# Kernel tuning notes

Hardware: AMD Instinct MI355X
Metric: run time of the kernel (lower is better)

## Reference

```python
import jax, jax.numpy as jnp
import numpy as np

B, N = 8, 256
IN_F, OUT_F = 64, 64
IN_E, OUT_E = 32, 64  # out_edges must equal out_features (batched matmul constraint)


def setup_inputs() -> dict:
    key = jax.random.key(0)
    ks = jax.random.split(key, 9)
    s = 0.05
    return {
        "A": jax.random.uniform(ks[0], (B, N, N), dtype=jnp.float32),
        "emb_node": jax.random.normal(ks[1], (B, N, IN_F), dtype=jnp.float32),
        "emb_edge": jax.random.normal(ks[2], (B, N, N, IN_E), dtype=jnp.float32),
        "W_node": jax.random.normal(ks[3], (IN_F, OUT_F), dtype=jnp.float32) * s,
        "b_node": jnp.zeros((OUT_F,), dtype=jnp.float32),
        "W_nodes": jax.random.normal(ks[4], (IN_F, OUT_F), dtype=jnp.float32) * s,
        "b_nodes": jnp.zeros((OUT_F,), dtype=jnp.float32),
        "W_edge": jax.random.normal(ks[5], (IN_E, OUT_E), dtype=jnp.float32) * s,
        "b_edge": jnp.zeros((OUT_E,), dtype=jnp.float32),
    }


def reference(A, emb_node, emb_edge, W_node, b_node, W_nodes, b_nodes, W_edge, b_edge):
    # Dense projections (last-axis matmul, like keras Dense)
    node_x = emb_node @ W_node + b_node        # [B,N,F]
    node_sx = emb_node @ W_nodes + b_nodes     # [B,N,F]
    edge_x = emb_edge @ W_edge + b_edge        # [B,N,N,E] (E == F)
    # Fused edge-weighted aggregation: original materializes A[...,None]*edge_x
    # then does a per-channel batched matmul with node_x; same math as:
    #   node_out[b,n,f] = sum_m A[b,n,m] * edge_x[b,n,m,f] * node_x[b,m,f]
    agg = jnp.einsum('bnm,bnmf,bmf->bnf', A, edge_x, node_x)
    node_out = jax.nn.relu(agg) + jax.nn.relu(node_sx)
    edge_out = jax.nn.relu(edge_x)
    return node_out, edge_out
```

## Files before the change

kernel.cpp:

```cpp
#include <hip/hip_runtime.h>

#define BB    8
#define NN    256
#define INF   64
#define OUTF  64
#define INE   32
#define OUTE  64

using f4 = __attribute__((ext_vector_type(4))) float;

__device__ float g_node_x[BB * NN * OUTF];
__device__ float g_relu_sx[BB * NN * OUTF];

__global__ __launch_bounds__(256) void node_proj(
    const float* __restrict__ emb_node,
    const float* __restrict__ W1, const float* __restrict__ b1,
    const float* __restrict__ W2, const float* __restrict__ b2)
{
    __shared__ float sW1[64][64];
    __shared__ float sW2[64][64];
    __shared__ float sE[4][64];

    const int tid = threadIdx.x;

    const f4* w1v = (const f4*)W1;
    const f4* w2v = (const f4*)W2;
    f4* s1 = (f4*)&sW1[0][0];
    f4* s2 = (f4*)&sW2[0][0];
#pragma unroll
    for (int i = 0; i < 4; ++i) {
        s1[tid + i * 256] = w1v[tid + i * 256];
        s2[tid + i * 256] = w2v[tid + i * 256];
    }
    const int row0 = blockIdx.x * 4;
    if (tid < 64) ((f4*)&sE[0][0])[tid] = ((const f4*)(emb_node + row0 * 64))[tid];
    __syncthreads();

    const int s = tid >> 6;
    const int f = tid & 63;
    float a1 = b1[f];
    float a2 = b2[f];
#pragma unroll
    for (int k = 0; k < 64; ++k) {
        const float e = sE[s][k];
        a1 = fmaf(e, sW1[k][f], a1);
        a2 = fmaf(e, sW2[k][f], a2);
    }
    const int row = row0 + s;
    g_node_x[row * 64 + f]  = a1;
    g_relu_sx[row * 64 + f] = fmaxf(a2, 0.f);
}

__global__ __launch_bounds__(512, 4) void edge_agg(
    const float* __restrict__ A,
    const float* __restrict__ emb_edge,
    const float* __restrict__ W_edge,
    const float* __restrict__ b_edge,
    float* __restrict__ node_out,
    float* __restrict__ edge_out)
{
    __shared__ float sE[256][36];
    __shared__ float sW[32][64];
    __shared__ float sA[256];
    __shared__ float sRed[32][64];

    const int tid = threadIdx.x;
    const int bn  = blockIdx.x;
    const int b   = bn >> 8;

    const float* embBase = emb_edge + (size_t)bn * (NN * INE);
#pragma unroll
    for (int it = 0; it < 4; ++it) {
        const int i  = tid + it * 512;
        const f4   v = __builtin_nontemporal_load(((const f4*)embBase) + i);
        const int m  = i >> 3;
        const int k4 = i & 7;
        *(f4*)&sE[m][k4 * 4] = v;
    }
    ((f4*)&sW[0][0])[tid] = ((const f4*)W_edge)[tid];
    if (tid < 64) ((f4*)sA)[tid] = ((const f4*)(A + bn * NN))[tid];
    __syncthreads();

    const int fg = tid & 15;
    const int mg = tid >> 4;
    const int f0 = fg * 4;

    const f4 bias = *(const f4*)(b_edge + f0);
    float acc[8][4];
#pragma unroll
    for (int i = 0; i < 8; ++i) {
        acc[i][0] = bias.x; acc[i][1] = bias.y; acc[i][2] = bias.z; acc[i][3] = bias.w;
    }

#pragma unroll
    for (int k4 = 0; k4 < 8; ++k4) {
        f4 ev[8];
#pragma unroll
        for (int i = 0; i < 8; ++i)
            ev[i] = *(const f4*)&sE[mg + i * 32][k4 * 4];
#pragma unroll
        for (int kk = 0; kk < 4; ++kk) {
            const f4 w = *(const f4*)&sW[k4 * 4 + kk][f0];
#pragma unroll
            for (int i = 0; i < 8; ++i) {
                const float e = (kk == 0) ? ev[i].x
                              : (kk == 1) ? ev[i].y
                              : (kk == 2) ? ev[i].z
                                          : ev[i].w;
                acc[i][0] = fmaf(e, w.x, acc[i][0]);
                acc[i][1] = fmaf(e, w.y, acc[i][1]);
                acc[i][2] = fmaf(e, w.z, acc[i][2]);
                acc[i][3] = fmaf(e, w.w, acc[i][3]);
            }
        }
    }

    const float* nx = g_node_x + b * (NN * OUTF);
    const size_t outBase = (size_t)bn * (NN * OUTE);
    float agg0 = 0.f, agg1 = 0.f, agg2 = 0.f, agg3 = 0.f;
#pragma unroll
    for (int i = 0; i < 8; ++i) {
        const int m = mg + i * 32;
        const float a = sA[m];
        const f4 nxv = *(const f4*)&nx[m * 64 + f0];
        f4 st;
        st.x = fmaxf(acc[i][0], 0.f);
        st.y = fmaxf(acc[i][1], 0.f);
        st.z = fmaxf(acc[i][2], 0.f);
        st.w = fmaxf(acc[i][3], 0.f);
        __builtin_nontemporal_store(st, (f4*)&edge_out[outBase + (size_t)m * 64 + f0]);
        agg0 = fmaf(a * acc[i][0], nxv.x, agg0);
        agg1 = fmaf(a * acc[i][1], nxv.y, agg1);
        agg2 = fmaf(a * acc[i][2], nxv.z, agg2);
        agg3 = fmaf(a * acc[i][3], nxv.w, agg3);
    }
    f4 aggv; aggv.x = agg0; aggv.y = agg1; aggv.z = agg2; aggv.w = agg3;
    *(f4*)&sRed[mg][f0] = aggv;
    __syncthreads();

    if (tid < 64) {
        float s = 0.f;
#pragma unroll
        for (int g = 0; g < 32; ++g) s += sRed[g][tid];
        node_out[bn * 64 + tid] = fmaxf(s, 0.f) + g_relu_sx[bn * 64 + tid];
    }
}

extern "C" void kernel_launch(void* const* d_in, const int* in_sizes, int n_in,
                              void* d_out, int out_size, void* d_ws, size_t ws_size,
                              hipStream_t stream) {
    const float* A        = (const float*)d_in[0];
    const float* emb_node = (const float*)d_in[1];
    const float* emb_edge = (const float*)d_in[2];
    const float* W_node   = (const float*)d_in[3];
    const float* b_node   = (const float*)d_in[4];
    const float* W_nodes  = (const float*)d_in[5];
    const float* b_nodes  = (const float*)d_in[6];
    const float* W_edge   = (const float*)d_in[7];
    const float* b_edge   = (const float*)d_in[8];

    float* node_out = (float*)d_out;
    float* edge_out = node_out + BB * NN * OUTF;

    node_proj<<<(BB * NN) / 4, 256, 0, stream>>>(emb_node, W_node, b_node, W_nodes, b_nodes);
    edge_agg<<<BB * NN, 512, 0, stream>>>(A, emb_edge, W_edge, b_edge, node_out, edge_out);
}
```

Before: 53.82 us.

## Compute edge projection with bf16 MFMA instead of FP32 FMAs

Converts the edge embeddings and a transposed copy of W_edge to bf16 in shared memory, then computes the 256x64 per-row projection with 16x16x32 bf16 MFMA instructions. The epilogue is restructured around the MFMA output layout: scalar nontemporal stores, and a wave-level shuffle reduction before a smaller cross-wave shared reduction. This is meant to cut ALU time and LDS traffic in the edge kernel. The risks are reduced precision from rounding inputs to bf16 and narrower store instructions.

```diff
diff --git a/kernel.cpp b/kernel.cpp
--- a/kernel.cpp
+++ b/kernel.cpp
@@ -7,10 +7,19 @@
 #define INE   32
 #define OUTE  64
 
-using f4 = __attribute__((ext_vector_type(4))) float;
+using f4     = __attribute__((ext_vector_type(4))) float;
+using f32x4  = __attribute__((ext_vector_type(4))) float;
+using bf16x8 = __attribute__((ext_vector_type(8))) short;
+using us4    = __attribute__((ext_vector_type(4))) unsigned short;
 
 __device__ float g_node_x[BB * NN * OUTF];
 __device__ float g_relu_sx[BB * NN * OUTF];
+
+static __device__ __forceinline__ unsigned short f2bf(float x) {
+    unsigned u = __builtin_bit_cast(unsigned, x);
+    u += 0x7fffu + ((u >> 16) & 1u);
+    return (unsigned short)(u >> 16);
+}
 
 __global__ __launch_bounds__(256) void node_proj(
     const float* __restrict__ emb_node,
@@ -59,89 +68,104 @@
     float* __restrict__ node_out,
     float* __restrict__ edge_out)
 {
-    __shared__ float sE[256][36];
-    __shared__ float sW[32][64];
+    __shared__ unsigned short sEb[256][32];
+    __shared__ unsigned short sWt[64][32];
     __shared__ float sA[256];
-    __shared__ float sRed[32][64];
+    __shared__ float sRed[8][64];
 
     const int tid = threadIdx.x;
     const int bn  = blockIdx.x;
     const int b   = bn >> 8;
 
-    const float* embBase = emb_edge + (size_t)bn * (NN * INE);
+    const f4* embv = (const f4*)(emb_edge + (size_t)bn * (NN * INE));
 #pragma unroll
     for (int it = 0; it < 4; ++it) {
-        const int i  = tid + it * 512;
-        const f4   v = __builtin_nontemporal_load(((const f4*)embBase) + i);
-        const int m  = i >> 3;
-        const int k4 = i & 7;
-        *(f4*)&sE[m][k4 * 4] = v;
+        const int i = tid + it * 512;
+        const f4 v = __builtin_nontemporal_load(embv + i);
+        us4 h;
+        h.x = f2bf(v.x); h.y = f2bf(v.y); h.z = f2bf(v.z); h.w = f2bf(v.w);
+        *(us4*)&sEb[i >> 3][(i & 7) * 4] = h;
     }
-    ((f4*)&sW[0][0])[tid] = ((const f4*)W_edge)[tid];
+    {
+        const int f  = tid >> 3;
+        const int k0 = (tid & 7) * 4;
+        us4 h;
+        h.x = f2bf(W_edge[(k0 + 0) * 64 + f]);
+        h.y = f2bf(W_edge[(k0 + 1) * 64 + f]);
+        h.z = f2bf(W_edge[(k0 + 2) * 64 + f]);
+        h.w = f2bf(W_edge[(k0 + 3) * 64 + f]);
+        *(us4*)&sWt[f][k0] = h;
+    }
     if (tid < 64) ((f4*)sA)[tid] = ((const f4*)(A + bn * NN))[tid];
+
+    const int wave  = tid >> 6;
+    const int lane  = tid & 63;
+    const int lrow  = lane >> 4;
+    const int lcol  = lane & 15;
+    const int mbase = wave * 32;
+
+    float bias[4];
+#pragma unroll
+    for (int ft = 0; ft < 4; ++ft) bias[ft] = b_edge[ft * 16 + lcol];
+
     __syncthreads();
 
-    const int fg = tid & 15;
-    const int mg = tid >> 4;
-    const int f0 = fg * 4;
+    bf16x8 afrag[2];
+#pragma unroll
+    for (int mt = 0; mt < 2; ++mt)
+        afrag[mt] = *(const bf16x8*)&sEb[mbase + mt * 16 + lcol][lrow * 8];
+    bf16x8 bfrag[4];
+#pragma unroll
+    for (int ft = 0; ft < 4; ++ft)
+        bfrag[ft] = *(const bf16x8*)&sWt[ft * 16 + lcol][lrow * 8];
 
-    const f4 bias = *(const f4*)(b_edge + f0);
-    float acc[8][4];
+    f32x4 acc[2][4];
 #pragma unroll
-    for (int i = 0; i < 8; ++i) {
-        acc[i][0] = bias.x; acc[i][1] = bias.y; acc[i][2] = bias.z; acc[i][3] = bias.w;
-    }
+    for (int mt = 0; mt < 2; ++mt)
+#pragma unroll
+        for (int ft = 0; ft < 4; ++ft) {
+            f32x4 c; c[0] = bias[ft]; c[1] = bias[ft]; c[2] = bias[ft]; c[3] = bias[ft];
+            acc[mt][ft] = __builtin_amdgcn_mfma_f32_16x16x32_bf16(
+                afrag[mt], bfrag[ft], c, 0, 0, 0);
+        }
 
+    const float* nx = g_node_x + b * (NN * OUTF);
+    float* eoutBase = edge_out + (size_t)bn * (NN * OUTE);
+    float agg[4] = {0.f, 0.f, 0.f, 0.f};
 #pragma unroll
-    for (int k4 = 0; k4 < 8; ++k4) {
-        f4 ev[8];
+    for (int mt = 0; mt < 2; ++mt) {
 #pragma unroll
-        for (int i = 0; i < 8; ++i)
-            ev[i] = *(const f4*)&sE[mg + i * 32][k4 * 4];
+        for (int r = 0; r < 4; ++r) {
+            const int m = mbase + mt * 16 + lrow * 4 + r;
+            const float a = sA[m];
+            const float* nxr = nx + m * 64 + lcol;
+            float* er = eoutBase + (size_t)m * 64 + lcol;
 #pragma unroll
-        for (int kk = 0; kk < 4; ++kk) {
-            const f4 w = *(const f4*)&sW[k4 * 4 + kk][f0];
-#pragma unroll
-            for (int i = 0; i < 8; ++i) {
-                const float e = (kk == 0) ? ev[i].x
-                              : (kk == 1) ? ev[i].y
-                              : (kk == 2) ? ev[i].z
-                                          : ev[i].w;
-                acc[i][0] = fmaf(e, w.x, acc[i][0]);
-                acc[i][1] = fmaf(e, w.y, acc[i][1]);
-                acc[i][2] = fmaf(e, w.z, acc[i][2]);
-                acc[i][3] = fmaf(e, w.w, acc[i][3]);
+            for (int ft = 0; ft < 4; ++ft) {
+                const float v = acc[mt][ft][r];
+                __builtin_nontemporal_store(fmaxf(v, 0.f), er + ft * 16);
+                agg[ft] = fmaf(a * v, nxr[ft * 16], agg[ft]);
             }
         }
     }
 
-    const float* nx = g_node_x + b * (NN * OUTF);
-    const size_t outBase = (size_t)bn * (NN * OUTE);
-    float agg0 = 0.f, agg1 = 0.f, agg2 = 0.f, agg3 = 0.f;
 #pragma unroll
-    for (int i = 0; i < 8; ++i) {
-        const int m = mg + i * 32;
-        const float a = sA[m];
-        const f4 nxv = *(const f4*)&nx[m * 64 + f0];
-        f4 st;
-        st.x = fmaxf(acc[i][0], 0.f);
-        st.y = fmaxf(acc[i][1], 0.f);
-        st.z = fmaxf(acc[i][2], 0.f);
-        st.w = fmaxf(acc[i][3], 0.f);
-        __builtin_nontemporal_store(st, (f4*)&edge_out[outBase + (size_t)m * 64 + f0]);
-        agg0 = fmaf(a * acc[i][0], nxv.x, agg0);
-        agg1 = fmaf(a * acc[i][1], nxv.y, agg1);
-        agg2 = fmaf(a * acc[i][2], nxv.z, agg2);
-        agg3 = fmaf(a * acc[i][3], nxv.w, agg3);
+    for (int ft = 0; ft < 4; ++ft) {
+        float v = agg[ft];
+        v += __shfl_xor(v, 16);
+        v += __shfl_xor(v, 32);
+        agg[ft] = v;
     }
-    f4 aggv; aggv.x = agg0; aggv.y = agg1; aggv.z = agg2; aggv.w = agg3;
-    *(f4*)&sRed[mg][f0] = aggv;
+    if (lane < 16) {
+#pragma unroll
+        for (int ft = 0; ft < 4; ++ft) sRed[wave][ft * 16 + lane] = agg[ft];
+    }
     __syncthreads();
 
     if (tid < 64) {
         float s = 0.f;
 #pragma unroll
-        for (int g = 0; g < 32; ++g) s += sRed[g][tid];
+        for (int w = 0; w < 8; ++w) s += sRed[w][tid];
         node_out[bn * 64 + tid] = fmaxf(s, 0.f) + g_relu_sx[bn * 64 + tid];
     }
 }
```

New measurement: 59.55 us. 1.11x slower.
